# Performance work log

Hardware: AMD Instinct MI355X
Metric: run time of the kernel (lower is better)

The kernel has to match this reference:

```python
import jax, jax.numpy as jnp
import numpy as np

N_NODES, N_EDGES, NHID = 50000, 1000000, 64
P = 2.0  # abs-power exponent


def setup_inputs() -> dict:
    key = jax.random.key(0)
    ks = jax.random.split(key, 7)
    X = jax.random.normal(ks[0], (N_NODES, NHID), dtype=jnp.float32)
    edge_index = jax.random.randint(ks[1], (2, N_EDGES), 0, N_NODES, dtype=jnp.int64)
    s1 = 1.0 / np.sqrt(NHID)
    W_self = jax.random.uniform(ks[2], (NHID, NHID), jnp.float32, -s1, s1)
    W_neigh = jax.random.uniform(ks[3], (NHID, NHID), jnp.float32, -s1, s1)
    b_sage = jax.random.uniform(ks[4], (NHID,), jnp.float32, -s1, s1)
    s2 = 1.0 / np.sqrt(2 * NHID)
    Q_w = jax.random.uniform(ks[5], (2 * NHID, NHID), jnp.float32, -s2, s2)
    Q_b = jax.random.uniform(ks[6], (NHID,), jnp.float32, -s2, s2)
    return {"X": X, "edge_index": edge_index, "W_self": W_self,
            "W_neigh": W_neigh, "b_sage": b_sage, "Q_w": Q_w, "Q_b": Q_b}


def _segment_mean(vals, ids, n):
    # scatter-mean with dim_size=n; empty segments -> 0 (matches torch_scatter 'mean')
    s = jax.ops.segment_sum(vals, ids, num_segments=n)
    cnt = jax.ops.segment_sum(jnp.ones((vals.shape[0], 1), vals.dtype), ids, num_segments=n)
    return s / jnp.maximum(cnt, 1.0)


def reference(X, edge_index, W_self, W_neigh, b_sage, Q_w, Q_b):
    n = X.shape[0]
    src, dst = edge_index[0], edge_index[1]
    # SAGEConv (mean aggregation): h_i = W_self x_i + W_neigh mean_{j->i} x_j + b
    mean_nb = _segment_mean(X[src], dst, n)                 # [N, nhid]
    H = jax.nn.relu(X @ W_self + mean_nb @ W_neigh + b_sage)  # activation(conv(X))
    # gather src/dst node feats, concat, small linear Q, |.|^p
    e = jnp.concatenate([H[src], H[dst]], axis=1) @ Q_w + Q_b  # [E, nhid]
    e = jnp.abs(e) ** P
    # scatter-mean keyed by edge src, then tanh
    return jnp.tanh(_segment_mean(e, src, n))               # [N, nhid]
```

## Files before the change

### kernel.cpp

```cpp
#include <hip/hip_runtime.h>
#include <math.h>

#define NN 50000
#define NE 1000000
#define NH 64
#define NKEY 100000
#define SPAN 512
#define NBKT 196
#define CAP 12288
#define CH 32

typedef _Float16 f16;
typedef _Float16 f16x4 __attribute__((ext_vector_type(4)));
typedef _Float16 f16x8 __attribute__((ext_vector_type(8)));
typedef float f32x4 __attribute__((ext_vector_type(4)));

__global__ __launch_bounds__(256) void pack_all(
    const float* __restrict__ X, f16* __restrict__ X16,
    const float* __restrict__ Ws, const float* __restrict__ Wn,
    const float* __restrict__ Qw, f16* __restrict__ wp) {
    int i = blockIdx.x * 256 + threadIdx.x;
    if (i < NN * NH / 4) {
        float4 v = ((const float4*)X)[i];
        f16x4 o = {(f16)v.x, (f16)v.y, (f16)v.z, (f16)v.w};
        ((f16x4*)X16)[i] = o;
    }
    if (i < 16384) {
        int m  = i >> 12;
        int kc = (i >> 11) & 1;
        int l  = (i >> 3) & 63;
        int e  = i & 7;
        int ct = (i >> 9) & 3;
        int k  = kc * 32 + (l >> 4) * 8 + e;
        int j  = ct * 16 + (l & 15);
        const float* W = (m == 0) ? Ws : (m == 1) ? Wn : (m == 2) ? Qw
                                                      : (Qw + 4096);
        wp[i] = (f16)W[k * 64 + j];
    }
}

__device__ __forceinline__ void push_pair(int key, int val, int* cnt,
                                          unsigned* buf, int* gcnt,
                                          unsigned* __restrict__ pairs) {
    int b = key >> 9;
    unsigned pk = ((unsigned)val << 9) | (unsigned)(key & 511);
    int slot = atomicAdd(&cnt[b], 1);
    if (slot < CH) {
        buf[b * CH + slot] = pk;
    } else {
        int g = atomicAdd(&gcnt[b], 1);
        if (g < CAP) pairs[(size_t)b * CAP + g] = pk;
    }
}

__device__ __forceinline__ void flush_coop(int* cnt, int* s_fc, int* s_g,
                                           unsigned* buf, int* gcnt,
                                           unsigned* __restrict__ pairs) {
    __syncthreads();
    int t = threadIdx.x;
    if (t < NBKT) {
        int fc = cnt[t]; if (fc > CH) fc = CH;
        s_fc[t] = fc;
        s_g[t] = (fc > 0) ? atomicAdd(&gcnt[t], fc) : 0;
    }
    __syncthreads();
    for (int i = t; i < NBKT * CH; i += 256) {
        int b = i >> 5, s = i & 31;
        if (s < s_fc[b])
            pairs[(size_t)b * CAP + s_g[b] + s] = buf[i];
    }
    __syncthreads();
    if (t < NBKT) cnt[t] = 0;
    __syncthreads();
}

__global__ __launch_bounds__(256) void bin_pass(
    const int* __restrict__ src, const int* __restrict__ dst,
    int* __restrict__ gcnt, unsigned* __restrict__ pairs) {
    __shared__ int cnt[NBKT];
    __shared__ int s_fc[NBKT];
    __shared__ int s_g[NBKT];
    __shared__ unsigned buf[NBKT * CH];
    for (int b = threadIdx.x; b < NBKT; b += 256) cnt[b] = 0;
    __syncthreads();
    int r = 0;
    for (int base = blockIdx.x * 256; base < NE; base += gridDim.x * 256) {
        int e = base + threadIdx.x;
        if (e < NE) {
            int s = src[e], d = dst[e];
            push_pair(s, d, cnt, buf, gcnt, pairs);
            push_pair(NN + d, s, cnt, buf, gcnt, pairs);
        }
        if ((++r & 7) == 0) flush_coop(cnt, s_fc, s_g, buf, gcnt, pairs);
    }
    flush_coop(cnt, s_fc, s_g, buf, gcnt, pairs);
}

__global__ __launch_bounds__(1024) void sort_pass(
    const unsigned* __restrict__ pairs, const int* __restrict__ gcnt,
    int* __restrict__ off, int* __restrict__ csr) {
    __shared__ int hist[SPAN];
    __shared__ int scn[SPAN];
    __shared__ int bsc[256];
    int k = blockIdx.x;
    int t = threadIdx.x;

    if (t < 256) bsc[t] = (t < NBKT) ? gcnt[t] : 0;
    __syncthreads();
    for (int o = 1; o < 256; o <<= 1) {
        int u = 0;
        if (t < 256 && t >= o) u = bsc[t - o];
        __syncthreads();
        if (t < 256) bsc[t] += u;
        __syncthreads();
    }
    int base = (k > 0) ? bsc[k - 1] : 0;
    int n = gcnt[k]; if (n > CAP) n = CAP;
    const unsigned* bp = pairs + (size_t)k * CAP;
    if (k == 0 && t == 0) off[NKEY] = 2 * NE;

    if (t < SPAN) hist[t] = 0;
    __syncthreads();
    for (int i = t; i < n; i += 1024)
        atomicAdd(&hist[bp[i] & 511], 1);
    __syncthreads();
    if (t < SPAN) scn[t] = hist[t];
    __syncthreads();
    for (int o = 1; o < SPAN; o <<= 1) {
        int u = 0;
        if (t < SPAN && t >= o) u = scn[t - o];
        __syncthreads();
        if (t < SPAN) scn[t] += u;
        __syncthreads();
    }
    if (t < SPAN) {
        int ex = base + scn[t] - hist[t];
        int gk = k * SPAN + t;
        if (gk < NKEY) off[gk] = ex;
        scn[t] = ex;
    }
    __syncthreads();
    for (int i = t; i < n; i += 1024) {
        unsigned p = bp[i];
        int pos = atomicAdd(&scn[p & 511], 1);
        csr[pos] = (int)(p >> 9);
    }
}

__device__ __forceinline__ int cidx(int i) {
    return max(0, min(i, NN - 1));
}

__device__ __forceinline__ float4 f16x4_to_f32(f16x4 r) {
    float4 o; o.x = (float)r.x; o.y = (float)r.y;
    o.z = (float)r.z; o.w = (float)r.w; return o;
}
__device__ __forceinline__ float4 shfl_xor4(float4 v, int m) {
    float4 o;
    o.x = __shfl_xor(v.x, m, 64); o.y = __shfl_xor(v.y, m, 64);
    o.z = __shfl_xor(v.z, m, 64); o.w = __shfl_xor(v.w, m, 64);
    return o;
}

__global__ __launch_bounds__(256) void gather_mean(
    const f16* __restrict__ X16, const int* __restrict__ off_dst,
    const int* __restrict__ csr, f16* __restrict__ M16) {
    int wid = (int)(((long long)blockIdx.x * blockDim.x + threadIdx.x) >> 6);
    int l = threadIdx.x & 63;
    int q = l & 15, g = l >> 4;
    if (wid >= NN) return;
    int e0 = off_dst[wid], e1 = off_dst[wid + 1];
    int deg = e1 - e0;
    const f16x4* Xq = (const f16x4*)(X16 + 4 * q);
    float4 s0 = {0,0,0,0}, s1 = {0,0,0,0}, s2 = {0,0,0,0}, s3 = {0,0,0,0};
    int Tf = deg >> 2;
    int t = 0;
    for (; t + 4 <= Tf; t += 4) {
        int i0 = cidx(csr[e0 + 4 * (t + 0) + g]);
        int i1 = cidx(csr[e0 + 4 * (t + 1) + g]);
        int i2 = cidx(csr[e0 + 4 * (t + 2) + g]);
        int i3 = cidx(csr[e0 + 4 * (t + 3) + g]);
        float4 r0 = f16x4_to_f32(Xq[(size_t)i0 * 16]);
        float4 r1 = f16x4_to_f32(Xq[(size_t)i1 * 16]);
        float4 r2 = f16x4_to_f32(Xq[(size_t)i2 * 16]);
        float4 r3 = f16x4_to_f32(Xq[(size_t)i3 * 16]);
        s0.x += r0.x; s0.y += r0.y; s0.z += r0.z; s0.w += r0.w;
        s1.x += r1.x; s1.y += r1.y; s1.z += r1.z; s1.w += r1.w;
        s2.x += r2.x; s2.y += r2.y; s2.z += r2.z; s2.w += r2.w;
        s3.x += r3.x; s3.y += r3.y; s3.z += r3.z; s3.w += r3.w;
    }
    for (; t < Tf; ++t) {
        int i0 = cidx(csr[e0 + 4 * t + g]);
        float4 r0 = f16x4_to_f32(Xq[(size_t)i0 * 16]);
        s0.x += r0.x; s0.y += r0.y; s0.z += r0.z; s0.w += r0.w;
    }
    int rem = deg & 3;
    if (rem) {
        int e = e0 + 4 * Tf + g;
        float m = (g < rem) ? 1.0f : 0.0f;
        int i0 = cidx(csr[(g < rem) ? e : (e1 - 1)]);
        float4 r0 = f16x4_to_f32(Xq[(size_t)i0 * 16]);
        s0.x += m * r0.x; s0.y += m * r0.y;
        s0.z += m * r0.z; s0.w += m * r0.w;
    }
    float4 s;
    s.x = (s0.x + s1.x) + (s2.x + s3.x);
    s.y = (s0.y + s1.y) + (s2.y + s3.y);
    s.z = (s0.z + s1.z) + (s2.z + s3.z);
    s.w = (s0.w + s1.w) + (s2.w + s3.w);
    float4 u = shfl_xor4(s, 16);
    s.x += u.x; s.y += u.y; s.z += u.z; s.w += u.w;
    u = shfl_xor4(s, 32);
    s.x += u.x; s.y += u.y; s.z += u.z; s.w += u.w;
    if (l < 16) {
        float inv = 1.0f / fmaxf((float)deg, 1.0f);
        f16x4 o = {(f16)(s.x * inv), (f16)(s.y * inv),
                   (f16)(s.z * inv), (f16)(s.w * inv)};
        *(f16x4*)&M16[(size_t)wid * NH + 4 * q] = o;
    }
}

__global__ __launch_bounds__(256) void node_gemm(
    const f16* __restrict__ X16, const f16* __restrict__ M16,
    const f16* __restrict__ wp, const float* __restrict__ bsage,
    float* __restrict__ A, f16* __restrict__ B16) {
    __shared__ f16 H16[64 * 64];
    const int T = threadIdx.x;
    const int l = T & 63, w = T >> 6;
    const int lr = l & 15, lg = l >> 4;
    const int nbase = blockIdx.x * 64;
    const int arow = w * 16 + lr;
    const int node = min(nbase + arow, NN - 1);
    const int kb = lg * 8;

    const f16x8* wv = (const f16x8*)wp;
    f16x8 xa0 = *(const f16x8*)&X16[(size_t)node * 64 + kb];
    f16x8 xa1 = *(const f16x8*)&X16[(size_t)node * 64 + 32 + kb];
    f16x8 ma0 = *(const f16x8*)&M16[(size_t)node * 64 + kb];
    f16x8 ma1 = *(const f16x8*)&M16[(size_t)node * 64 + 32 + kb];

    #pragma unroll
    for (int ct = 0; ct < 4; ++ct) {
        f16x8 ws0 = wv[(0 + ct) * 64 + l];
        f16x8 ws1 = wv[(4 + ct) * 64 + l];
        f16x8 wn0 = wv[(8 + ct) * 64 + l];
        f16x8 wn1 = wv[(12 + ct) * 64 + l];
        float bj = bsage[ct * 16 + lr];
        f32x4 acc = {bj, bj, bj, bj};
        acc = __builtin_amdgcn_mfma_f32_16x16x32_f16(xa0, ws0, acc, 0, 0, 0);
        acc = __builtin_amdgcn_mfma_f32_16x16x32_f16(xa1, ws1, acc, 0, 0, 0);
        acc = __builtin_amdgcn_mfma_f32_16x16x32_f16(ma0, wn0, acc, 0, 0, 0);
        acc = __builtin_amdgcn_mfma_f32_16x16x32_f16(ma1, wn1, acc, 0, 0, 0);
        #pragma unroll
        for (int i = 0; i < 4; ++i) {
            int rr = w * 16 + lg * 4 + i;
            int cc = ct * 16 + lr;
            H16[rr * 64 + ((((cc >> 3) ^ (rr & 7)) << 3) | (cc & 7))] =
                (f16)fmaxf(acc[i], 0.0f);
        }
    }
    __syncthreads();

    f16x8 ha0 = *(const f16x8*)
        &H16[arow * 64 + (((kb >> 3) ^ (arow & 7)) << 3)];
    f16x8 ha1 = *(const f16x8*)
        &H16[arow * 64 + ((((kb + 32) >> 3) ^ (arow & 7)) << 3)];
    #pragma unroll
    for (int ct = 0; ct < 4; ++ct) {
        f16x8 q10 = wv[(16 + ct) * 64 + l];
        f16x8 q11 = wv[(20 + ct) * 64 + l];
        f16x8 q20 = wv[(24 + ct) * 64 + l];
        f16x8 q21 = wv[(28 + ct) * 64 + l];
        f32x4 aA = {0.f, 0.f, 0.f, 0.f};
        f32x4 aB = {0.f, 0.f, 0.f, 0.f};
        aA = __builtin_amdgcn_mfma_f32_16x16x32_f16(ha0, q10, aA, 0, 0, 0);
        aA = __builtin_amdgcn_mfma_f32_16x16x32_f16(ha1, q11, aA, 0, 0, 0);
        aB = __builtin_amdgcn_mfma_f32_16x16x32_f16(ha0, q20, aB, 0, 0, 0);
        aB = __builtin_amdgcn_mfma_f32_16x16x32_f16(ha1, q21, aB, 0, 0, 0);
        #pragma unroll
        for (int i = 0; i < 4; ++i) {
            int gr = nbase + w * 16 + lg * 4 + i;
            if (gr < NN) {
                int cc = ct * 16 + lr;
                A[(size_t)gr * 64 + cc] = aA[i];
                B16[(size_t)gr * 64 + cc] = (f16)aB[i];
            }
        }
    }
}

__global__ __launch_bounds__(256) void edge_out(
    const float* __restrict__ A, const f16* __restrict__ B16,
    const float* __restrict__ Qb, const int* __restrict__ off_src,
    const int* __restrict__ csr, float* __restrict__ out) {
    int wid = (int)(((long long)blockIdx.x * blockDim.x + threadIdx.x) >> 6);
    int l = threadIdx.x & 63;
    int q = l & 15, g = l >> 4;
    if (wid >= NN) return;
    float4 aq = *(const float4*)&A[(size_t)wid * NH + 4 * q];
    float4 qb = *(const float4*)&Qb[4 * q];
    aq.x += qb.x; aq.y += qb.y; aq.z += qb.z; aq.w += qb.w;
    int e0 = off_src[wid], e1 = off_src[wid + 1];
    int deg = e1 - e0;
    const f16x4* Bq = (const f16x4*)(B16 + 4 * q);
    float4 s0 = {0,0,0,0}, s1 = {0,0,0,0}, s2 = {0,0,0,0}, s3 = {0,0,0,0};
    int Tf = deg >> 2;
    int t = 0;
#define EACC(sv, rv)                                                   \
    { float4 tv;                                                       \
      tv.x = aq.x + rv.x; tv.y = aq.y + rv.y;                          \
      tv.z = aq.z + rv.z; tv.w = aq.w + rv.w;                          \
      sv.x += tv.x * tv.x; sv.y += tv.y * tv.y;                        \
      sv.z += tv.z * tv.z; sv.w += tv.w * tv.w; }
    for (; t + 4 <= Tf; t += 4) {
        int i0 = cidx(csr[e0 + 4 * (t + 0) + g]);
        int i1 = cidx(csr[e0 + 4 * (t + 1) + g]);
        int i2 = cidx(csr[e0 + 4 * (t + 2) + g]);
        int i3 = cidx(csr[e0 + 4 * (t + 3) + g]);
        float4 r0 = f16x4_to_f32(Bq[(size_t)i0 * 16]);
        float4 r1 = f16x4_to_f32(Bq[(size_t)i1 * 16]);
        float4 r2 = f16x4_to_f32(Bq[(size_t)i2 * 16]);
        float4 r3 = f16x4_to_f32(Bq[(size_t)i3 * 16]);
        EACC(s0, r0) EACC(s1, r1) EACC(s2, r2) EACC(s3, r3)
    }
    for (; t < Tf; ++t) {
        int i0 = cidx(csr[e0 + 4 * t + g]);
        float4 r0 = f16x4_to_f32(Bq[(size_t)i0 * 16]);
        EACC(s0, r0)
    }
    int rem = deg & 3;
    if (rem) {
        int e = e0 + 4 * Tf + g;
        float m = (g < rem) ? 1.0f : 0.0f;
        int i0 = cidx(csr[(g < rem) ? e : (e1 - 1)]);
        float4 r0 = f16x4_to_f32(Bq[(size_t)i0 * 16]);
        float4 tv;
        tv.x = aq.x + r0.x; tv.y = aq.y + r0.y;
        tv.z = aq.z + r0.z; tv.w = aq.w + r0.w;
        s0.x += m * tv.x * tv.x; s0.y += m * tv.y * tv.y;
        s0.z += m * tv.z * tv.z; s0.w += m * tv.w * tv.w;
    }
#undef EACC
    float4 s;
    s.x = (s0.x + s1.x) + (s2.x + s3.x);
    s.y = (s0.y + s1.y) + (s2.y + s3.y);
    s.z = (s0.z + s1.z) + (s2.z + s3.z);
    s.w = (s0.w + s1.w) + (s2.w + s3.w);
    float4 u = shfl_xor4(s, 16);
    s.x += u.x; s.y += u.y; s.z += u.z; s.w += u.w;
    u = shfl_xor4(s, 32);
    s.x += u.x; s.y += u.y; s.z += u.z; s.w += u.w;
    if (l < 16) {
        float inv = 1.0f / fmaxf((float)deg, 1.0f);
        float4 o;
        o.x = tanhf(s.x * inv); o.y = tanhf(s.y * inv);
        o.z = tanhf(s.z * inv); o.w = tanhf(s.w * inv);
        *(float4*)&out[(size_t)wid * NH + 4 * q] = o;
    }
}

extern "C" void kernel_launch(void* const* d_in, const int* in_sizes, int n_in,
                              void* d_out, int out_size, void* d_ws, size_t ws_size,
                              hipStream_t stream) {
    const float* X      = (const float*)d_in[0];
    const int*   ei     = (const int*)d_in[1];
    const float* Wself  = (const float*)d_in[2];
    const float* Wneigh = (const float*)d_in[3];
    const float* bsage  = (const float*)d_in[4];
    const float* Qw     = (const float*)d_in[5];
    const float* Qb     = (const float*)d_in[6];
    const int* src = ei;
    const int* dst = ei + NE;

    float* out = (float*)d_out;

    float* A   = (float*)d_ws;
    f16* X16   = (f16*)(A + (size_t)NN * NH);
    f16* B16   = X16 + (size_t)NN * NH;
    unsigned* pairs = (unsigned*)(B16 + (size_t)NN * NH);
    f16* M16   = (f16*)pairs;
    int* csr   = (int*)(pairs + (size_t)NBKT * CAP);
    int* off   = csr + 2 * NE;
    int* gcnt  = off + NKEY + 1;
    f16* wp    = (f16*)(gcnt + NBKT);

    hipMemsetAsync(gcnt, 0, NBKT * sizeof(int), stream);

    pack_all<<<(NN * NH / 4 + 255) / 256, 256, 0, stream>>>(X, X16, Wself,
                                                            Wneigh, Qw, wp);
    bin_pass<<<512, 256, 0, stream>>>(src, dst, gcnt, pairs);
    sort_pass<<<NBKT, 1024, 0, stream>>>(pairs, gcnt, off, csr);
    gather_mean<<<(NN + 3) / 4, 256, 0, stream>>>(X16, off + NN, csr, M16);
    node_gemm<<<(NN + 63) / 64, 256, 0, stream>>>(X16, M16, wp, bsage, A, B16);
    edge_out<<<(NN + 3) / 4, 256, 0, stream>>>(A, B16, Qb, off, csr, out);
}
```

Measured before the change: 124.1 us.

## Fuse X/weight packing into bin pass and neighbor mean into node GEMM

The fp16 packing of X and the weights now runs in extra blocks of the binning kernel, so that work shares a launch with the binning and can overlap it. The neighbor-mean gather is moved into the node GEMM kernel, which builds each 64-node tile's mean rows in a swizzled shared-memory tile. This removes the M16 round trip through global memory and two kernel launches. In exchange, each wave now walks 16 nodes one after another, which lowers gather parallelism: 782 blocks instead of 12500 waves-of-4, and the load is less balanced across nodes with different degrees.

```diff
diff --git a/kernel.cpp b/kernel.cpp
--- a/kernel.cpp
+++ b/kernel.cpp
@@ -9,35 +9,13 @@
 #define NBKT 196
 #define CAP 12288
 #define CH 32
+#define BINB 512
+#define PACKB 256
 
 typedef _Float16 f16;
 typedef _Float16 f16x4 __attribute__((ext_vector_type(4)));
 typedef _Float16 f16x8 __attribute__((ext_vector_type(8)));
 typedef float f32x4 __attribute__((ext_vector_type(4)));
-
-__global__ __launch_bounds__(256) void pack_all(
-    const float* __restrict__ X, f16* __restrict__ X16,
-    const float* __restrict__ Ws, const float* __restrict__ Wn,
-    const float* __restrict__ Qw, f16* __restrict__ wp) {
-    int i = blockIdx.x * 256 + threadIdx.x;
-    if (i < NN * NH / 4) {
-        float4 v = ((const float4*)X)[i];
-        f16x4 o = {(f16)v.x, (f16)v.y, (f16)v.z, (f16)v.w};
-        ((f16x4*)X16)[i] = o;
-    }
-    if (i < 16384) {
-        int m  = i >> 12;
-        int kc = (i >> 11) & 1;
-        int l  = (i >> 3) & 63;
-        int e  = i & 7;
-        int ct = (i >> 9) & 3;
-        int k  = kc * 32 + (l >> 4) * 8 + e;
-        int j  = ct * 16 + (l & 15);
-        const float* W = (m == 0) ? Ws : (m == 1) ? Wn : (m == 2) ? Qw
-                                                      : (Qw + 4096);
-        wp[i] = (f16)W[k * 64 + j];
-    }
-}
 
 __device__ __forceinline__ void push_pair(int key, int val, int* cnt,
                                           unsigned* buf, int* gcnt,
@@ -76,7 +54,31 @@
 
 __global__ __launch_bounds__(256) void bin_pass(
     const int* __restrict__ src, const int* __restrict__ dst,
-    int* __restrict__ gcnt, unsigned* __restrict__ pairs) {
+    int* __restrict__ gcnt, unsigned* __restrict__ pairs,
+    const float* __restrict__ X, f16* __restrict__ X16,
+    const float* __restrict__ Ws, const float* __restrict__ Wn,
+    const float* __restrict__ Qw, f16* __restrict__ wp) {
+    if (blockIdx.x >= BINB) {
+        int start = (blockIdx.x - BINB) * 256 + threadIdx.x;
+        for (int i = start; i < NN * NH / 4; i += PACKB * 256) {
+            float4 v = ((const float4*)X)[i];
+            f16x4 o = {(f16)v.x, (f16)v.y, (f16)v.z, (f16)v.w};
+            ((f16x4*)X16)[i] = o;
+        }
+        for (int i = start; i < 16384; i += PACKB * 256) {
+            int m  = i >> 12;
+            int kc = (i >> 11) & 1;
+            int l  = (i >> 3) & 63;
+            int e  = i & 7;
+            int ct = (i >> 9) & 3;
+            int k  = kc * 32 + (l >> 4) * 8 + e;
+            int j  = ct * 16 + (l & 15);
+            const float* W = (m == 0) ? Ws : (m == 1) ? Wn : (m == 2) ? Qw
+                                                          : (Qw + 4096);
+            wp[i] = (f16)W[k * 64 + j];
+        }
+        return;
+    }
     __shared__ int cnt[NBKT];
     __shared__ int s_fc[NBKT];
     __shared__ int s_g[NBKT];
@@ -84,7 +86,7 @@
     for (int b = threadIdx.x; b < NBKT; b += 256) cnt[b] = 0;
     __syncthreads();
     int r = 0;
-    for (int base = blockIdx.x * 256; base < NE; base += gridDim.x * 256) {
+    for (int base = blockIdx.x * 256; base < NE; base += BINB * 256) {
         int e = base + threadIdx.x;
         if (e < NE) {
             int s = src[e], d = dst[e];
@@ -162,73 +164,75 @@
     return o;
 }
 
-__global__ __launch_bounds__(256) void gather_mean(
+__global__ __launch_bounds__(256) void node_gemm(
     const f16* __restrict__ X16, const int* __restrict__ off_dst,
-    const int* __restrict__ csr, f16* __restrict__ M16) {
-    int wid = (int)(((long long)blockIdx.x * blockDim.x + threadIdx.x) >> 6);
-    int l = threadIdx.x & 63;
-    int q = l & 15, g = l >> 4;
-    if (wid >= NN) return;
-    int e0 = off_dst[wid], e1 = off_dst[wid + 1];
-    int deg = e1 - e0;
-    const f16x4* Xq = (const f16x4*)(X16 + 4 * q);
-    float4 s0 = {0,0,0,0}, s1 = {0,0,0,0}, s2 = {0,0,0,0}, s3 = {0,0,0,0};
-    int Tf = deg >> 2;
-    int t = 0;
-    for (; t + 4 <= Tf; t += 4) {
-        int i0 = cidx(csr[e0 + 4 * (t + 0) + g]);
-        int i1 = cidx(csr[e0 + 4 * (t + 1) + g]);
-        int i2 = cidx(csr[e0 + 4 * (t + 2) + g]);
-        int i3 = cidx(csr[e0 + 4 * (t + 3) + g]);
-        float4 r0 = f16x4_to_f32(Xq[(size_t)i0 * 16]);
-        float4 r1 = f16x4_to_f32(Xq[(size_t)i1 * 16]);
-        float4 r2 = f16x4_to_f32(Xq[(size_t)i2 * 16]);
-        float4 r3 = f16x4_to_f32(Xq[(size_t)i3 * 16]);
-        s0.x += r0.x; s0.y += r0.y; s0.z += r0.z; s0.w += r0.w;
-        s1.x += r1.x; s1.y += r1.y; s1.z += r1.z; s1.w += r1.w;
-        s2.x += r2.x; s2.y += r2.y; s2.z += r2.z; s2.w += r2.w;
-        s3.x += r3.x; s3.y += r3.y; s3.z += r3.z; s3.w += r3.w;
-    }
-    for (; t < Tf; ++t) {
-        int i0 = cidx(csr[e0 + 4 * t + g]);
-        float4 r0 = f16x4_to_f32(Xq[(size_t)i0 * 16]);
-        s0.x += r0.x; s0.y += r0.y; s0.z += r0.z; s0.w += r0.w;
-    }
-    int rem = deg & 3;
-    if (rem) {
-        int e = e0 + 4 * Tf + g;
-        float m = (g < rem) ? 1.0f : 0.0f;
-        int i0 = cidx(csr[(g < rem) ? e : (e1 - 1)]);
-        float4 r0 = f16x4_to_f32(Xq[(size_t)i0 * 16]);
-        s0.x += m * r0.x; s0.y += m * r0.y;
-        s0.z += m * r0.z; s0.w += m * r0.w;
-    }
-    float4 s;
-    s.x = (s0.x + s1.x) + (s2.x + s3.x);
-    s.y = (s0.y + s1.y) + (s2.y + s3.y);
-    s.z = (s0.z + s1.z) + (s2.z + s3.z);
-    s.w = (s0.w + s1.w) + (s2.w + s3.w);
-    float4 u = shfl_xor4(s, 16);
-    s.x += u.x; s.y += u.y; s.z += u.z; s.w += u.w;
-    u = shfl_xor4(s, 32);
-    s.x += u.x; s.y += u.y; s.z += u.z; s.w += u.w;
-    if (l < 16) {
-        float inv = 1.0f / fmaxf((float)deg, 1.0f);
-        f16x4 o = {(f16)(s.x * inv), (f16)(s.y * inv),
-                   (f16)(s.z * inv), (f16)(s.w * inv)};
-        *(f16x4*)&M16[(size_t)wid * NH + 4 * q] = o;
-    }
-}
-
-__global__ __launch_bounds__(256) void node_gemm(
-    const f16* __restrict__ X16, const f16* __restrict__ M16,
-    const f16* __restrict__ wp, const float* __restrict__ bsage,
-    float* __restrict__ A, f16* __restrict__ B16) {
+    const int* __restrict__ csr, const f16* __restrict__ wp,
+    const float* __restrict__ bsage, float* __restrict__ A,
+    f16* __restrict__ B16) {
     __shared__ f16 H16[64 * 64];
+    __shared__ f16 Mt[64 * 64];
     const int T = threadIdx.x;
     const int l = T & 63, w = T >> 6;
+    const int nbase = blockIdx.x * 64;
+    const int q = l & 15, g = l >> 4;
+
+    const f16x4* Xq = (const f16x4*)(X16 + 4 * q);
+    for (int nn = 0; nn < 16; ++nn) {
+        int lrow = w * 16 + nn;
+        int wid = min(nbase + lrow, NN - 1);
+        int e0 = off_dst[wid], e1 = off_dst[wid + 1];
+        int deg = e1 - e0;
+        float4 s0 = {0,0,0,0}, s1 = {0,0,0,0}, s2 = {0,0,0,0}, s3 = {0,0,0,0};
+        int Tf = deg >> 2;
+        int t = 0;
+        for (; t + 4 <= Tf; t += 4) {
+            int i0 = cidx(csr[e0 + 4 * (t + 0) + g]);
+            int i1 = cidx(csr[e0 + 4 * (t + 1) + g]);
+            int i2 = cidx(csr[e0 + 4 * (t + 2) + g]);
+            int i3 = cidx(csr[e0 + 4 * (t + 3) + g]);
+            float4 r0 = f16x4_to_f32(Xq[(size_t)i0 * 16]);
+            float4 r1 = f16x4_to_f32(Xq[(size_t)i1 * 16]);
+            float4 r2 = f16x4_to_f32(Xq[(size_t)i2 * 16]);
+            float4 r3 = f16x4_to_f32(Xq[(size_t)i3 * 16]);
+            s0.x += r0.x; s0.y += r0.y; s0.z += r0.z; s0.w += r0.w;
+            s1.x += r1.x; s1.y += r1.y; s1.z += r1.z; s1.w += r1.w;
+            s2.x += r2.x; s2.y += r2.y; s2.z += r2.z; s2.w += r2.w;
+            s3.x += r3.x; s3.y += r3.y; s3.z += r3.z; s3.w += r3.w;
+        }
+        for (; t < Tf; ++t) {
+            int i0 = cidx(csr[e0 + 4 * t + g]);
+            float4 r0 = f16x4_to_f32(Xq[(size_t)i0 * 16]);
+            s0.x += r0.x; s0.y += r0.y; s0.z += r0.z; s0.w += r0.w;
+        }
+        int rem = deg & 3;
+        if (rem) {
+            int e = e0 + 4 * Tf + g;
+            float m = (g < rem) ? 1.0f : 0.0f;
+            int i0 = cidx(csr[(g < rem) ? e : (e1 - 1)]);
+            float4 r0 = f16x4_to_f32(Xq[(size_t)i0 * 16]);
+            s0.x += m * r0.x; s0.y += m * r0.y;
+            s0.z += m * r0.z; s0.w += m * r0.w;
+        }
+        float4 s;
+        s.x = (s0.x + s1.x) + (s2.x + s3.x);
+        s.y = (s0.y + s1.y) + (s2.y + s3.y);
+        s.z = (s0.z + s1.z) + (s2.z + s3.z);
+        s.w = (s0.w + s1.w) + (s2.w + s3.w);
+        float4 u = shfl_xor4(s, 16);
+        s.x += u.x; s.y += u.y; s.z += u.z; s.w += u.w;
+        u = shfl_xor4(s, 32);
+        s.x += u.x; s.y += u.y; s.z += u.z; s.w += u.w;
+        if (l < 16) {
+            float inv = 1.0f / fmaxf((float)deg, 1.0f);
+            f16x4 o = {(f16)(s.x * inv), (f16)(s.y * inv),
+                       (f16)(s.z * inv), (f16)(s.w * inv)};
+            *(f16x4*)&Mt[lrow * 64 + ((((q >> 1) ^ (lrow & 7)) << 3) |
+                                      ((q & 1) << 2))] = o;
+        }
+    }
+    __syncthreads();
+
     const int lr = l & 15, lg = l >> 4;
-    const int nbase = blockIdx.x * 64;
     const int arow = w * 16 + lr;
     const int node = min(nbase + arow, NN - 1);
     const int kb = lg * 8;
@@ -236,8 +240,9 @@
     const f16x8* wv = (const f16x8*)wp;
     f16x8 xa0 = *(const f16x8*)&X16[(size_t)node * 64 + kb];
     f16x8 xa1 = *(const f16x8*)&X16[(size_t)node * 64 + 32 + kb];
-    f16x8 ma0 = *(const f16x8*)&M16[(size_t)node * 64 + kb];
-    f16x8 ma1 = *(const f16x8*)&M16[(size_t)node * 64 + 32 + kb];
+    f16x8 ma0 = *(const f16x8*)&Mt[arow * 64 + (((kb >> 3) ^ (arow & 7)) << 3)];
+    f16x8 ma1 = *(const f16x8*)
+        &Mt[arow * 64 + ((((kb + 32) >> 3) ^ (arow & 7)) << 3)];
 
     #pragma unroll
     for (int ct = 0; ct < 4; ++ct) {
@@ -378,7 +383,6 @@
     f16* X16   = (f16*)(A + (size_t)NN * NH);
     f16* B16   = X16 + (size_t)NN * NH;
     unsigned* pairs = (unsigned*)(B16 + (size_t)NN * NH);
-    f16* M16   = (f16*)pairs;
     int* csr   = (int*)(pairs + (size_t)NBKT * CAP);
     int* off   = csr + 2 * NE;
     int* gcnt  = off + NKEY + 1;
@@ -386,11 +390,10 @@
 
     hipMemsetAsync(gcnt, 0, NBKT * sizeof(int), stream);
 
-    pack_all<<<(NN * NH / 4 + 255) / 256, 256, 0, stream>>>(X, X16, Wself,
-                                                            Wneigh, Qw, wp);
-    bin_pass<<<512, 256, 0, stream>>>(src, dst, gcnt, pairs);
+    bin_pass<<<BINB + PACKB, 256, 0, stream>>>(src, dst, gcnt, pairs,
+                                               X, X16, Wself, Wneigh, Qw, wp);
     sort_pass<<<NBKT, 1024, 0, stream>>>(pairs, gcnt, off, csr);
-    gather_mean<<<(NN + 3) / 4, 256, 0, stream>>>(X16, off + NN, csr, M16);
-    node_gemm<<<(NN + 63) / 64, 256, 0, stream>>>(X16, M16, wp, bsage, A, B16);
+    node_gemm<<<(NN + 63) / 64, 256, 0, stream>>>(X16, off + NN, csr, wp,
+                                                  bsage, A, B16);
     edge_out<<<(NN + 3) / 4, 256, 0, stream>>>(A, B16, Qb, off, csr, out);
 }
```

After: 134.8 us. +8.6%, slower.
